# Performance work log

Measured on AMD Instinct MI355X. Metric: run time of the kernel, lower is better.

The kernel has to match this reference:

```python
import jax, jax.numpy as jnp
import numpy as np

B, N, NPOINT, NSAMPLE = 8, 8192, 2048, 32
RADIUS = 0.4
C_IN = 64
MLP = [64, 64, 128]
EPS = 1e-5
BIG = 1e10


def setup_inputs() -> dict:
    key = jax.random.key(0)
    ks = jax.random.split(key, 2 + 4 * len(MLP))
    inp = {
        'xyz': jax.random.normal(ks[0], (B, N, 3), jnp.float32),
        'features': jax.random.normal(ks[1], (B, C_IN, N), jnp.float32),
    }
    last_c = C_IN + 3
    j = 2
    for i, out_c in enumerate(MLP):
        inp[f'w{i}'] = jax.random.normal(ks[j], (out_c, last_c), jnp.float32) * (1.0 / np.sqrt(last_c)); j += 1
        inp[f'b{i}'] = jax.random.normal(ks[j], (out_c,), jnp.float32) * 0.01; j += 1
        inp[f'g{i}'] = 1.0 + 0.01 * jax.random.normal(ks[j], (out_c,), jnp.float32); j += 1
        inp[f'bt{i}'] = 0.01 * jax.random.normal(ks[j], (out_c,), jnp.float32); j += 1
        last_c = out_c
    return inp


def fps(xyz, m):
    # Farthest point sampling; deterministic start at index 0 (torch uses randint).
    b, n, _ = xyz.shape

    def step(carry, _):
        dist, far = carry
        centroid = jnp.take_along_axis(xyz, far[:, None, None], axis=1)  # [B,1,3]
        d = jnp.sum((xyz - centroid) ** 2, axis=-1)                      # [B,N]
        dist = jnp.minimum(dist, d)
        new_far = jnp.argmax(dist, axis=1)
        return (dist, new_far), far

    init = (jnp.full((b, n), BIG, xyz.dtype), jnp.zeros((b,), jnp.int32))
    _, idxs = jax.lax.scan(step, init, None, length=m)
    return jnp.transpose(idxs)  # [B,m]


def ball_query(xyz, centroids, radius, k):
    # Euclidean cdist via the (a-b)^2 = a^2 + b^2 - 2ab expansion.
    x2 = jnp.sum(xyz * xyz, axis=-1)            # [B,N]
    c2 = jnp.sum(centroids * centroids, axis=-1)  # [B,M]
    d2 = c2[:, :, None] + x2[:, None, :] - 2.0 * jnp.einsum('bmd,bnd->bmn', centroids, xyz)
    d = jnp.sqrt(jnp.maximum(d2, 0.0))           # [B,M,N]
    dm = jnp.where(d <= radius, d, BIG)
    _, idx = jax.lax.top_k(-dm, k)               # k smallest distances
    return idx                                   # [B,M,K]


def gather_points(x, idx):
    # x: [B,N,C], idx: [B,M,K] -> [B,M,K,C]
    b = x.shape[0]
    return x[jnp.arange(b)[:, None, None], idx]


def reference(xyz, features, w0, b0, g0, bt0, w1, b1, g1, bt1, w2, b2, g2, bt2):
    idx = fps(xyz, NPOINT)                                   # [B,M]
    new_xyz = jnp.take_along_axis(xyz, idx[:, :, None], axis=1)  # [B,M,3]
    knn_idx = ball_query(xyz, new_xyz, RADIUS, NSAMPLE)      # [B,M,K]
    grouped_xyz = gather_points(xyz, knn_idx)                # [B,M,K,3]
    grouped_xyz_norm = grouped_xyz - new_xyz[:, :, None, :]
    grouped_feat = gather_points(jnp.transpose(features, (0, 2, 1)), knn_idx)  # [B,M,K,C]
    feat = jnp.concatenate([grouped_xyz_norm, grouped_feat], axis=-1)          # [B,M,K,C+3]

    for w, b, g, bt in ((w0, b0, g0, bt0), (w1, b1, g1, bt1), (w2, b2, g2, bt2)):
        feat = jnp.einsum('bmkc,oc->bmko', feat, w) + b      # 1x1 conv
        mu = jnp.mean(feat, axis=(0, 1, 2))                  # BN, training-mode batch stats
        var = jnp.mean((feat - mu) ** 2, axis=(0, 1, 2))
        feat = (feat - mu) * jax.lax.rsqrt(var + EPS) * g + bt
        feat = jax.nn.relu(feat)

    new_feat = jnp.max(feat, axis=2)                         # max over neighbors -> [B,M,C_out]
    return new_xyz, jnp.transpose(new_feat, (0, 2, 1))       # [B,M,3], [B,C_out,M]
```

## Files before the change

### kernel.cpp

```cpp
#include <hip/hip_runtime.h>
#include <hip/hip_bf16.h>
#include <stdint.h>

typedef unsigned short u16;
typedef unsigned int   u32;
typedef unsigned long long u64;
typedef float v2f __attribute__((ext_vector_type(2)));
typedef __attribute__((ext_vector_type(8))) short bf16x8;
typedef __attribute__((ext_vector_type(4))) float f32x4;

#define B_    8
#define N_    8192
#define M_    2048
#define NS_   32
#define CIN_  64
#define ROWS_ (B_*M_*NS_)
#define BIGF  1e10f
#define EPSF  1e-5f
#define INV_ROWS (1.0f/524288.0f)

__device__ __forceinline__ u16 f2bf(float f){
  u32 x=__float_as_uint(f);
  return (u16)((x + 0x7FFFu + ((x>>16)&1u))>>16);
}
__device__ __forceinline__ float bf2f(u16 u){ return __uint_as_float(((u32)u)<<16); }

__device__ __forceinline__ u64 wave_max_key(u64 k){
#define DPP_LVL(CTRL) { \
    u32 lo_=(u32)__builtin_amdgcn_update_dpp(0,(int)(u32)k,(CTRL),0xF,0xF,true); \
    u32 hi_=(u32)__builtin_amdgcn_update_dpp(0,(int)(u32)(k>>32),(CTRL),0xF,0xF,true); \
    u64 o_=((u64)hi_<<32)|(u64)lo_; \
    k=(o_>k)?o_:k; }
  DPP_LVL(0x111)
  DPP_LVL(0x112)
  DPP_LVL(0x114)
  DPP_LVL(0x118)
  DPP_LVL(0x142)
  DPP_LVL(0x143)
#undef DPP_LVL
  return k;
}

__global__ __launch_bounds__(256) void k_prep(
    const float* w0,const float* b0,const float* g0,const float* bt0,
    const float* w1,const float* b1,const float* g1,const float* bt1,
    const float* w2,const float* b2,const float* g2,const float* bt2,
    float* biasf,float* gf,float* btf,float* stats,
    u16* Wb0h, u16* Wb0l, u16* Wb1h, u16* Wb1l, u16* Wb2h, u16* Wb2l)
{
  int tid=threadIdx.x;
  for (int i=tid;i<768;i+=256) stats[i]=0.f;
  for (int i=tid;i<6144;i+=256){
    int e=i&7, lane=(i>>3)&63, idx=i>>9;
    int tn=idx/3, k0=idx%3;
    int col = tn*16 + (lane&15);
    int k   = k0*32 + ((lane>>4)&3)*8 + e;
    float v = 0.f;
    if (k < 64)            v = w0[col*67 + 3 + k];
    else if (k < 67)       v = w0[col*67 + (k-64)];
    u16 hib = f2bf(v);
    Wb0h[i] = hib;
    Wb0l[i] = f2bf(v - bf2f(hib));
  }
  for (int i=tid;i<4096;i+=256){
    int e=i&7, lane=(i>>3)&63, k0=(i>>9)&1, tn=i>>10;
    int col = tn*16 + (lane&15);
    int k   = k0*32 + ((lane>>4)&3)*8 + e;
    float v = w1[col*64 + k];
    u16 hib = f2bf(v);
    Wb1h[i] = hib;
    Wb1l[i] = f2bf(v - bf2f(hib));
  }
  for (int i=tid;i<8192;i+=256){
    int e=i&7, lane=(i>>3)&63, k0=(i>>9)&1, tn=i>>10;
    int col = tn*16 + (lane&15);
    int k   = k0*32 + ((lane>>4)&3)*8 + e;
    float v = w2[col*64 + k];
    u16 hib = f2bf(v);
    Wb2h[i] = hib;
    Wb2l[i] = f2bf(v - bf2f(hib));
  }
  if (tid<64){
    biasf[0*128+tid]=b0[tid]; gf[0*128+tid]=g0[tid]; btf[0*128+tid]=bt0[tid];
    biasf[1*128+tid]=b1[tid]; gf[1*128+tid]=g1[tid]; btf[1*128+tid]=bt1[tid];
  }
  if (tid<128){
    biasf[2*128+tid]=b2[tid]; gf[2*128+tid]=g2[tid]; btf[2*128+tid]=bt2[tid];
  }
}

__global__ __launch_bounds__(512) void k_fpstr(const float* __restrict__ xyz,
                                               float* __restrict__ nxyz, float* __restrict__ out0,
                                               const float* __restrict__ feats, u16* __restrict__ featT)
{
#pragma clang fp contract(off)
  __shared__ float sx[N_], sy[N_], sz[N_];
  __shared__ int sidx[M_];
  __shared__ u64 skey[2][8];
  int tid=threadIdx.x;
  if (blockIdx.x >= 8){
    float (*t)[65] = (float(*)[65])sx;
    int idx = blockIdx.x - 8;
    int bb = idx >> 7, n0 = (idx & 127) * 64;
    int a=tid&63, q=tid>>6;
    const float* fp = feats + (size_t)bb*CIN_*N_;
    #pragma unroll
    for (int s=0;s<8;s++){ int c=q*8+s; t[c][a]=fp[(size_t)c*N_ + n0 + a]; }
    __syncthreads();
    u16* op = featT + (size_t)bb*N_*CIN_;
    #pragma unroll
    for (int s=0;s<8;s++){ int n=q*8+s; op[(size_t)(n0+n)*CIN_ + a] = f2bf(t[a][n]); }
    return;
  }
  int b=blockIdx.x;
  const float* xp = xyz + (size_t)b*N_*3;
  for (int i=tid;i<N_;i+=512){ sx[i]=xp[i*3]; sy[i]=xp[i*3+1]; sz[i]=xp[i*3+2]; }
  __syncthreads();
  v2f px[8],py[8],pz[8],md[8];
  int base = tid*16;
  #pragma unroll
  for (int p=0;p<8;p++){
    px[p]=*(const v2f*)&sx[base+2*p];
    py[p]=*(const v2f*)&sy[base+2*p];
    pz[p]=*(const v2f*)&sz[base+2*p];
    v2f m0; m0[0]=BIGF; m0[1]=BIGF; md[p]=m0;
  }
  u32 invb = 0xFFFFFFFFu - (u32)base;
  int far=0;
  int lane=tid&63, wv=tid>>6;
  for (int step=0; step<M_; step++){
    if (tid==0) sidx[step]=far;
    float cxs=sx[far], cys=sy[far], czs=sz[far];
    v2f cx; cx[0]=cxs; cx[1]=cxs;
    v2f cy; cy[0]=cys; cy[1]=cys;
    v2f cz; cz[0]=czs; cz[1]=czs;
    u64 kb=0;
    #pragma unroll
    for (int p=0;p<8;p++){
      v2f dx=px[p]-cx, dy=py[p]-cy, dz=pz[p]-cz;
      v2f d=(dx*dx+dy*dy)+dz*dz;
      v2f m=__builtin_elementwise_min(md[p],d);
      md[p]=m;
      u64 k0=((u64)__float_as_uint(m[0])<<32)|(u64)(invb-(u32)(2*p));
      u64 k1=((u64)__float_as_uint(m[1])<<32)|(u64)(invb-(u32)(2*p+1));
      u64 kp=(k1>k0)?k1:k0;
      kb=(kp>kb)?kp:kb;
    }
    kb = wave_max_key(kb);
    int par = step & 1;
    if (lane==63) skey[par][wv]=kb;
    __syncthreads();
    u64 a0=skey[par][0],a1=skey[par][1],a2=skey[par][2],a3=skey[par][3];
    u64 a4=skey[par][4],a5=skey[par][5],a6=skey[par][6],a7=skey[par][7];
    a0=(a1>a0)?a1:a0; a2=(a3>a2)?a3:a2; a4=(a5>a4)?a5:a4; a6=(a7>a6)?a7:a6;
    a0=(a2>a0)?a2:a0; a4=(a6>a4)?a6:a4;
    a0=(a4>a0)?a4:a0;
    far = (int)(0xFFFFFFFFu - (u32)(a0 & 0xFFFFFFFFull));
  }
  for (int i=tid;i<M_;i+=512){
    int id = sidx[i];
    float x=sx[id], y=sy[id], z=sz[id];
    size_t o=(size_t)(b*M_+i)*3;
    nxyz[o]=x; nxyz[o+1]=y; nxyz[o+2]=z;
    out0[o]=x; out0[o+1]=y; out0[o+2]=z;
  }
}

#define BQCAP 512
__global__ __launch_bounds__(512) void k_bq(const float* __restrict__ xyz, const float* __restrict__ nxyz,
                                            int* __restrict__ knn)
{
  __shared__ float4 sP[N_];
  __shared__ float candd[8][BQCAP];
  __shared__ u16  candi[8][BQCAP];
  int tid=threadIdx.x;
  int cid0 = blockIdx.x*8;
  int b = cid0 >> 11;
  const float* xp = xyz + (size_t)b*N_*3;
  for (int i=tid;i<N_;i+=512){
    float x=xp[i*3], y=xp[i*3+1], z=xp[i*3+2];
    float x2 = __fmul_rn(x,x);
    x2 = __fadd_rn(x2, __fmul_rn(y,y));
    x2 = __fadd_rn(x2, __fmul_rn(z,z));
    sP[i]=make_float4(x,y,z,x2);
  }
  __syncthreads();
  int w=tid>>6, lane=tid&63;
  int cid = cid0 + w;
  float cx=nxyz[(size_t)cid*3], cy=nxyz[(size_t)cid*3+1], cz=nxyz[(size_t)cid*3+2];
  float c2 = __fmul_rn(cx,cx);
  c2 = __fadd_rn(c2, __fmul_rn(cy,cy));
  c2 = __fadd_rn(c2, __fmul_rn(cz,cz));
  int cnt=0;
  for (int i0=0;i0<N_;i0+=64){
    int i=i0+lane;
    float4 p=sP[i];
    float dot = __fmul_rn(cx,p.x);
    dot = __fadd_rn(dot, __fmul_rn(cy,p.y));
    dot = __fadd_rn(dot, __fmul_rn(cz,p.z));
    float d2 = __fsub_rn(__fadd_rn(c2,p.w), __fmul_rn(2.0f,dot));
    float d = sqrtf(fmaxf(d2,0.f));
    bool in = (d <= 0.4f);
    u64 msk = __ballot(in);
    int pos = cnt + __popcll(msk & ((1ull<<lane)-1ull));
    if (in && pos<BQCAP){ candd[w][pos]=d; candi[w][pos]=(u16)i; }
    cnt += __popcll(msk);
  }
  int R = cnt<BQCAP ? cnt : BQCAP;
  int* kout = knn + (size_t)cid*NS_;
  if (R >= NS_){
    for (int s=0;s<NS_;s++){
      u64 kb = ~0ull;
      for (int j=lane;j<R;j+=64){
        float v=candd[w][j];
        u64 k = ((u64)__float_as_uint(v)<<32) | (u64)(u32)j;
        kb = (k<kb)?k:kb;
      }
      u64 inv = wave_max_key(~kb);
      if (lane==63){
        u64 kw = ~inv;
        int bpp = (int)(u32)(kw & 0xFFFFFFFFull);
        kout[s]=candi[w][bpp];
        candd[w][bpp]=3e38f;
      }
    }
  } else {
    if (lane<R) kout[lane]=candi[w][lane];
    int need = NS_-R, slot = R;
    for (int i0=0; i0<N_ && need>0; i0+=64){
      int i=i0+lane;
      float4 p=sP[i];
      float dot = __fmul_rn(cx,p.x);
      dot = __fadd_rn(dot, __fmul_rn(cy,p.y));
      dot = __fadd_rn(dot, __fmul_rn(cz,p.z));
      float d2 = __fsub_rn(__fadd_rn(c2,p.w), __fmul_rn(2.0f,dot));
      float d = sqrtf(fmaxf(d2,0.f));
      bool in = (d <= 0.4f);
      u64 mm = __ballot(!in);
      while (mm && need>0){
        int bpos = __ffsll((long long)mm)-1;
        if (lane==0) kout[slot] = i0+bpos;
        slot++; need--;
        mm &= mm-1;
      }
    }
  }
}

__global__ __launch_bounds__(256) void k_mm0(const float* __restrict__ xyz, const u16* __restrict__ featT,
                                             const int* __restrict__ knn, const float* __restrict__ nxyz,
                                             const u16* __restrict__ Wb0h, const u16* __restrict__ Wb0l,
                                             const float* __restrict__ bias0, u16* __restrict__ Y0)
{
  __shared__ u16 Xs[64*128];
  __shared__ u16 WH[12*64*8];
  __shared__ u16 WL[12*64*8];
  int tid=threadIdx.x;
  {
    const uint4* s4=(const uint4*)Wb0h; uint4* d4=(uint4*)WH;
    const uint4* s5=(const uint4*)Wb0l; uint4* d5=(uint4*)WL;
    for (int i=tid;i<768;i+=256){ d4[i]=s4[i]; d5[i]=s5[i]; }
  }
  size_t base=(size_t)blockIdx.x*64;
  {
    int rl=tid>>2, t=tid&3;
    int row=(int)base+rl;
    int bm = row>>5, b = row>>16;
    int n  = knn[row];
    const uint4* fp = (const uint4*)(featT + ((size_t)b*N_ + n)*CIN_);
    char* xr = (char*)Xs + rl*256;
    u32 swz = (u32)((rl&7)<<4);
    uint4 v0=fp[t*2], v1=fp[t*2+1];
    *(uint4*)(xr + ((t*32)    ^ swz)) = v0;
    *(uint4*)(xr + ((t*32+16) ^ swz)) = v1;
    uint4 pz = make_uint4(0u,0u,0u,0u);
    if (t==0){
      const float* cp = nxyz + (size_t)bm*3;
      const float* xp = xyz + ((size_t)b*N_ + n)*3;
      u32 w01 = (u32)f2bf(xp[0]-cp[0]) | ((u32)f2bf(xp[1]-cp[1])<<16);
      u32 w2  = (u32)f2bf(xp[2]-cp[2]);
      pz.x = w01; pz.y = w2;
    }
    *(uint4*)(xr + ((128+t*16) ^ swz)) = pz;
  }
  __syncthreads();
  int w=tid>>6, lane=tid&63;
  f32x4 acc[4];
  #pragma unroll
  for (int tn=0;tn<4;tn++){ acc[tn][0]=0.f; acc[tn][1]=0.f; acc[tn][2]=0.f; acc[tn][3]=0.f; }
  int arow = w*16 + (lane&15);
  u32 aswz = (u32)((arow&7)<<4);
  #pragma unroll
  for (int k0=0;k0<3;k0++){
    int aoff = arow*256 + (int)(((u32)((k0*32 + ((lane>>4)&3)*8)*2)) ^ aswz);
    bf16x8 a = *(const bf16x8*)((const char*)Xs + aoff);
    #pragma unroll
    for (int tn=0;tn<4;tn++){
      bf16x8 bl = *(const bf16x8*)&WL[((tn*3+k0)*64+lane)*8];
      bf16x8 bh = *(const bf16x8*)&WH[((tn*3+k0)*64+lane)*8];
      acc[tn] = __builtin_amdgcn_mfma_f32_16x16x32_bf16(a, bl, acc[tn], 0,0,0);
      acc[tn] = __builtin_amdgcn_mfma_f32_16x16x32_bf16(a, bh, acc[tn], 0,0,0);
    }
  }
  #pragma unroll
  for (int tn=0;tn<4;tn++){
    int col = tn*16 + (lane&15);
    float bb = bias0[col];
    #pragma unroll
    for (int j=0;j<4;j++){
      int row = w*16 + (lane>>4)*4 + j;
      Y0[(base+row)*64 + col] = f2bf(acc[tn][j] + bb);
    }
  }
}

template<int C>
__global__ __launch_bounds__(256) void k_stats(const u16* __restrict__ Y, float* __restrict__ statsOut)
{
  __shared__ float sred[4][128];
  int tid=threadIdx.x;
  int c0=(tid&7)*8;
  int rg=tid>>3;
  float s[8], ss[8];
  #pragma unroll
  for (int k=0;k<8;k++){ s[k]=0.f; ss[k]=0.f; }
  for (size_t r=(size_t)blockIdx.x*32+rg; r<ROWS_; r+=(size_t)gridDim.x*32){
    uint4 v=*(const uint4*)&Y[r*64+c0];
    u32 a[4]={v.x,v.y,v.z,v.w};
    #pragma unroll
    for (int q=0;q<4;q++){
      float lo=bf2f((u16)(a[q]&0xFFFFu));
      float hi=bf2f((u16)(a[q]>>16));
      s[q*2]+=lo;   ss[q*2]+=lo*lo;
      s[q*2+1]+=hi; ss[q*2+1]+=hi*hi;
    }
  }
  #pragma unroll
  for (int off=32; off>=8; off>>=1){
    #pragma unroll
    for (int k=0;k<8;k++){
      s[k]+=__shfl_down(s[k],off);
      ss[k]+=__shfl_down(ss[k],off);
    }
  }
  int lane=tid&63, wv=tid>>6;
  if (lane<8){
    #pragma unroll
    for (int k=0;k<8;k++){
      int ch=lane*8+k;
      sred[wv][ch]=s[k];
      sred[wv][64+ch]=ss[k];
    }
  }
  __syncthreads();
  if (tid<128){
    float a=sred[0][tid]+sred[1][tid]+sred[2][tid]+sred[3][tid];
    int ch=tid&63, which=tid>>6;
    atomicAdd(&statsOut[ch*2+which], a);
  }
}

__global__ __launch_bounds__(256) void k_mm1(u16* __restrict__ Y,
                                             const u16* __restrict__ Wb1h, const u16* __restrict__ Wb1l,
                                             const float* __restrict__ bias1, const float* __restrict__ gf0,
                                             const float* __restrict__ btf0, const float* __restrict__ stats0)
{
  __shared__ u16 Xs[64*64];
  __shared__ u16 WH[8*64*8];
  __shared__ u16 WL[8*64*8];
  __shared__ float sc[64], sh[64];
  int tid=threadIdx.x;
  if (tid<64){
    float mu = stats0[tid*2]*INV_ROWS;
    float var= stats0[tid*2+1]*INV_ROWS - mu*mu;
    float rs = 1.0f/sqrtf(var+EPSF);
    float s  = rs*gf0[tid];
    sc[tid]=s; sh[tid]=btf0[tid]-mu*s;
  }
  {
    const uint4* sh4=(const uint4*)Wb1h; uint4* dh4=(uint4*)WH;
    const uint4* sl4=(const uint4*)Wb1l; uint4* dl4=(uint4*)WL;
    dh4[tid]=sh4[tid]; dh4[tid+256]=sh4[tid+256];
    dl4[tid]=sl4[tid]; dl4[tid+256]=sl4[tid+256];
  }
  __syncthreads();
  size_t base=(size_t)blockIdx.x*64;
  for (int i=tid;i<512;i+=256){
    int rl=i>>3, c0=(i&7)*8;
    uint4 v=*(const uint4*)(Y + (base+rl)*64 + c0);
    u32 arr[4]={v.x,v.y,v.z,v.w};
    u32 pk[4];
    #pragma unroll
    for (int q=0;q<4;q++){
      int cc=c0+q*2;
      float lo=bf2f((u16)(arr[q]&0xFFFFu));
      float hi=bf2f((u16)(arr[q]>>16));
      lo=fmaxf(0.f, lo*sc[cc]+sh[cc]);
      hi=fmaxf(0.f, hi*sc[cc+1]+sh[cc+1]);
      pk[q] = (u32)f2bf(lo) | ((u32)f2bf(hi)<<16);
    }
    uint4 o4; o4.x=pk[0]; o4.y=pk[1]; o4.z=pk[2]; o4.w=pk[3];
    int byteoff = rl*128 + ((c0*2) ^ ((rl&7)<<4));
    *(uint4*)((char*)Xs + byteoff) = o4;
  }
  __syncthreads();
  int w=tid>>6, lane=tid&63;
  f32x4 acc[4];
  #pragma unroll
  for (int tn=0;tn<4;tn++){ acc[tn][0]=0.f; acc[tn][1]=0.f; acc[tn][2]=0.f; acc[tn][3]=0.f; }
  int arow = w*16 + (lane&15);
  #pragma unroll
  for (int k0=0;k0<2;k0++){
    int aoff = arow*128 + ((k0*64 + (lane>>4)*16) ^ ((arow&7)<<4));
    bf16x8 a = *(const bf16x8*)((const char*)Xs + aoff);
    #pragma unroll
    for (int tn=0;tn<4;tn++){
      bf16x8 bl = *(const bf16x8*)&WL[((tn*2+k0)*64+lane)*8];
      bf16x8 bh = *(const bf16x8*)&WH[((tn*2+k0)*64+lane)*8];
      acc[tn] = __builtin_amdgcn_mfma_f32_16x16x32_bf16(a, bl, acc[tn], 0,0,0);
      acc[tn] = __builtin_amdgcn_mfma_f32_16x16x32_bf16(a, bh, acc[tn], 0,0,0);
    }
  }
  #pragma unroll
  for (int tn=0;tn<4;tn++){
    int col = tn*16 + (lane&15);
    float bb = bias1[col];
    #pragma unroll
    for (int j=0;j<4;j++){
      int row = w*16 + (lane>>4)*4 + j;
      Y[(base+row)*64 + col] = f2bf(acc[tn][j] + bb);
    }
  }
}

__global__ __launch_bounds__(256) void k_mm2a(const u16* __restrict__ Y1,
                                              const u16* __restrict__ Wb2h, const u16* __restrict__ Wb2l,
                                              const float* __restrict__ bias2, const float* __restrict__ gf1,
                                              const float* __restrict__ btf1, const float* __restrict__ stats1,
                                              float* __restrict__ stats2, float* __restrict__ out1)
{
  __shared__ u16 Xs[64*64];
  __shared__ u16 WH[8192];
  __shared__ u16 WL[8192];
  __shared__ float Ys[64*128];
  __shared__ float sc[64], sh[64];
  __shared__ float sred[512];
  int tid=threadIdx.x;
  if (tid<64){
    float mu = stats1[tid*2]*INV_ROWS;
    float var= stats1[tid*2+1]*INV_ROWS - mu*mu;
    float rs = 1.0f/sqrtf(var+EPSF);
    float s  = rs*gf1[tid];
    sc[tid]=s; sh[tid]=btf1[tid]-mu*s;
  }
  {
    const uint4* s4=(const uint4*)Wb2h; uint4* d4=(uint4*)WH;
    const uint4* s5=(const uint4*)Wb2l; uint4* d5=(uint4*)WL;
    for (int i=tid;i<1024;i+=256){ d4[i]=s4[i]; d5[i]=s5[i]; }
  }
  int w=tid>>6, lane=tid&63;
  int pg=tid>>7, po=tid&127;
  float accSum=0.f, accSq=0.f;
  __syncthreads();
  for (int tile=blockIdx.x; tile<8192; tile+=gridDim.x){
    size_t base=(size_t)tile*64;
    for (int i=tid;i<512;i+=256){
      int rl=i>>3, c0=(i&7)*8;
      uint4 v=*(const uint4*)(Y1 + (base+rl)*64 + c0);
      u32 arr[4]={v.x,v.y,v.z,v.w};
      u32 pk[4];
      #pragma unroll
      for (int q=0;q<4;q++){
        int cc=c0+q*2;
        float lo=bf2f((u16)(arr[q]&0xFFFFu));
        float hi=bf2f((u16)(arr[q]>>16));
        lo=fmaxf(0.f, lo*sc[cc]+sh[cc]);
        hi=fmaxf(0.f, hi*sc[cc+1]+sh[cc+1]);
        pk[q] = (u32)f2bf(lo) | ((u32)f2bf(hi)<<16);
      }
      uint4 o4; o4.x=pk[0]; o4.y=pk[1]; o4.z=pk[2]; o4.w=pk[3];
      int byteoff = rl*128 + ((c0*2) ^ ((rl&7)<<4));
      *(uint4*)((char*)Xs + byteoff) = o4;
    }
    __syncthreads();
    f32x4 acc[8];
    #pragma unroll
    for (int tn=0;tn<8;tn++){ acc[tn][0]=0.f; acc[tn][1]=0.f; acc[tn][2]=0.f; acc[tn][3]=0.f; }
    int arow = w*16 + (lane&15);
    #pragma unroll
    for (int k0=0;k0<2;k0++){
      int aoff = arow*128 + ((k0*64 + (lane>>4)*16) ^ ((arow&7)<<4));
      bf16x8 a = *(const bf16x8*)((const char*)Xs + aoff);
      #pragma unroll
      for (int tn=0;tn<8;tn++){
        bf16x8 bl = *(const bf16x8*)&WL[((tn*2+k0)*64+lane)*8];
        bf16x8 bh = *(const bf16x8*)&WH[((tn*2+k0)*64+lane)*8];
        acc[tn] = __builtin_amdgcn_mfma_f32_16x16x32_bf16(a, bl, acc[tn], 0,0,0);
        acc[tn] = __builtin_amdgcn_mfma_f32_16x16x32_bf16(a, bh, acc[tn], 0,0,0);
      }
    }
    #pragma unroll
    for (int tn=0;tn<8;tn++){
      int col = tn*16 + (lane&15);
      float bb = bias2[col];
      #pragma unroll
      for (int j=0;j<4;j++){
        int row = w*16 + (lane>>4)*4 + j;
        int byteoff = row*512 + ((col*4) ^ ((row&7)<<4));
        *(float*)((char*)Ys + byteoff) = acc[tn][j] + bb;
      }
    }
    __syncthreads();
    {
      float mx=-3e38f;
      #pragma unroll 4
      for (int k=0;k<32;k++){
        int row = pg*32 + k;
        int byteoff = row*512 + ((po*4) ^ ((row&7)<<4));
        float y = *(const float*)((const char*)Ys + byteoff);
        accSum += y; accSq += y*y;
        mx = fmaxf(mx, y);
      }
      int bm = tile*2 + pg; int bi = bm>>11, m = bm&2047;
      out1[((size_t)bi*128+po)*M_ + m] = mx;
    }
    __syncthreads();
  }
  sred[tid]      = accSum;
  sred[256+tid]  = accSq;
  __syncthreads();
  if (tid<128){
    float s = sred[tid] + sred[tid+128];
    float q = sred[256+tid] + sred[256+tid+128];
    atomicAdd(&stats2[tid*2],   s);
    atomicAdd(&stats2[tid*2+1], q);
  }
}

__global__ __launch_bounds__(256) void k_pool(float* __restrict__ out1, const float* __restrict__ stats2,
                                              const float* __restrict__ gf2, const float* __restrict__ btf2)
{
  int idx = blockIdx.x*256 + threadIdx.x;
  int o = (idx >> 11) & 127;
  float mu = stats2[o*2]*INV_ROWS;
  float var= stats2[o*2+1]*INV_ROWS - mu*mu;
  float rs = 1.0f/sqrtf(var+EPSF);
  float s  = rs*gf2[o];
  float sh = btf2[o]-mu*s;
  out1[idx] = fmaxf(0.f, out1[idx]*s + sh);
}

extern "C" void kernel_launch(void* const* d_in, const int* in_sizes, int n_in,
                              void* d_out, int out_size, void* d_ws, size_t ws_size,
                              hipStream_t stream)
{
  (void)in_sizes; (void)n_in; (void)out_size; (void)ws_size;
  const float* xyz =(const float*)d_in[0];
  const float* feat=(const float*)d_in[1];
  const float* w0=(const float*)d_in[2],  *b0=(const float*)d_in[3],  *g0=(const float*)d_in[4],  *bt0=(const float*)d_in[5];
  const float* w1=(const float*)d_in[6],  *b1=(const float*)d_in[7],  *g1=(const float*)d_in[8],  *bt1=(const float*)d_in[9];
  const float* w2=(const float*)d_in[10], *b2=(const float*)d_in[11], *g2=(const float*)d_in[12], *bt2=(const float*)d_in[13];
  float* out0=(float*)d_out;
  float* out1=out0 + (size_t)B_*M_*3;

  char* ws=(char*)d_ws;
  float* nxyz =(float*)(ws);
  u16*   Wb1h =(u16*)  (ws + 196608);
  u16*   Wb1l =(u16*)  (ws + 204800);
  u16*   Wb2h =(u16*)  (ws + 212992);
  u16*   Wb2l =(u16*)  (ws + 229376);
  int*   knn  =(int*)  (ws + 262144);
  u16*   Wb0h =(u16*)  (ws + 2359296);
  u16*   Wb0l =(u16*)  (ws + 2376704);
  float* biasf=(float*)(ws + 2425856);
  float* gfp  =(float*)(ws + 2427392);
  float* btfp =(float*)(ws + 2428928);
  float* stats=(float*)(ws + 2430464);
  u16*   featT=(u16*)  (ws + 2433536);
  u16*   Y0   =(u16*)  (ws + 10822144);

  k_prep<<<1,256,0,stream>>>(w0,b0,g0,bt0,w1,b1,g1,bt1,w2,b2,g2,bt2,biasf,gfp,btfp,stats,
                             Wb0h,Wb0l,Wb1h,Wb1l,Wb2h,Wb2l);
  k_fpstr<<<8+1024,512,0,stream>>>(xyz, nxyz, out0, feat, featT);
  k_bq<<<2048,512,0,stream>>>(xyz, nxyz, knn);
  k_mm0<<<8192,256,0,stream>>>(xyz, featT, knn, nxyz, Wb0h, Wb0l, biasf+0, Y0);
  k_stats<64><<<128,256,0,stream>>>(Y0, stats+0);
  k_mm1<<<8192,256,0,stream>>>(Y0, Wb1h, Wb1l, biasf+128, gfp+0, btfp+0, stats+0);
  k_stats<64><<<128,256,0,stream>>>(Y0, stats+256);
  k_mm2a<<<512,256,0,stream>>>(Y0, Wb2h, Wb2l, biasf+256, gfp+128, btfp+128, stats+256, stats+512, out1);
  k_pool<<<8192,256,0,stream>>>(out1, stats+512, gfp+256, btfp+256);
}
```

Baseline: 2.323 ms.

## Fuse BN stats into matmul kernels, persistent grids, drop LDS staging in ball query

The two standalone batch-norm statistics kernels are removed. Their per-channel sum and sum-of-squares are now accumulated in the epilogues of k_mm0 and k_mm1, which become persistent 512-block grids looping over tiles, with shared-memory then global atomics for the totals. This saves two full re-reads of the intermediate activation buffer and two launches. Separately, k_bq no longer stages all 8192 points in LDS and instead reads xyz directly from global memory, recomputing |p|^2 per point. That lowers LDS use and may raise occupancy, at the cost of uncoalesced stride-3 global loads in the hot loop.

Measured after the change: 2.186 ms. 1.06x faster.

```diff
diff --git a/kernel.cpp b/kernel.cpp
--- a/kernel.cpp
+++ b/kernel.cpp
@@ -170,21 +170,12 @@
 __global__ __launch_bounds__(512) void k_bq(const float* __restrict__ xyz, const float* __restrict__ nxyz,
                                             int* __restrict__ knn)
 {
-  __shared__ float4 sP[N_];
   __shared__ float candd[8][BQCAP];
   __shared__ u16  candi[8][BQCAP];
   int tid=threadIdx.x;
   int cid0 = blockIdx.x*8;
   int b = cid0 >> 11;
   const float* xp = xyz + (size_t)b*N_*3;
-  for (int i=tid;i<N_;i+=512){
-    float x=xp[i*3], y=xp[i*3+1], z=xp[i*3+2];
-    float x2 = __fmul_rn(x,x);
-    x2 = __fadd_rn(x2, __fmul_rn(y,y));
-    x2 = __fadd_rn(x2, __fmul_rn(z,z));
-    sP[i]=make_float4(x,y,z,x2);
-  }
-  __syncthreads();
   int w=tid>>6, lane=tid&63;
   int cid = cid0 + w;
   float cx=nxyz[(size_t)cid*3], cy=nxyz[(size_t)cid*3+1], cz=nxyz[(size_t)cid*3+2];
@@ -194,11 +185,14 @@
   int cnt=0;
   for (int i0=0;i0<N_;i0+=64){
     int i=i0+lane;
-    float4 p=sP[i];
-    float dot = __fmul_rn(cx,p.x);
-    dot = __fadd_rn(dot, __fmul_rn(cy,p.y));
-    dot = __fadd_rn(dot, __fmul_rn(cz,p.z));
-    float d2 = __fsub_rn(__fadd_rn(c2,p.w), __fmul_rn(2.0f,dot));
+    float x=xp[i*3], y=xp[i*3+1], z=xp[i*3+2];
+    float pw = __fmul_rn(x,x);
+    pw = __fadd_rn(pw, __fmul_rn(y,y));
+    pw = __fadd_rn(pw, __fmul_rn(z,z));
+    float dot = __fmul_rn(cx,x);
+    dot = __fadd_rn(dot, __fmul_rn(cy,y));
+    dot = __fadd_rn(dot, __fmul_rn(cz,z));
+    float d2 = __fsub_rn(__fadd_rn(c2,pw), __fmul_rn(2.0f,dot));
     float d = sqrtf(fmaxf(d2,0.f));
     bool in = (d <= 0.4f);
     u64 msk = __ballot(in);
@@ -229,11 +223,14 @@
     int need = NS_-R, slot = R;
     for (int i0=0; i0<N_ && need>0; i0+=64){
       int i=i0+lane;
-      float4 p=sP[i];
-      float dot = __fmul_rn(cx,p.x);
-      dot = __fadd_rn(dot, __fmul_rn(cy,p.y));
-      dot = __fadd_rn(dot, __fmul_rn(cz,p.z));
-      float d2 = __fsub_rn(__fadd_rn(c2,p.w), __fmul_rn(2.0f,dot));
+      float x=xp[i*3], y=xp[i*3+1], z=xp[i*3+2];
+      float pw = __fmul_rn(x,x);
+      pw = __fadd_rn(pw, __fmul_rn(y,y));
+      pw = __fadd_rn(pw, __fmul_rn(z,z));
+      float dot = __fmul_rn(cx,x);
+      dot = __fadd_rn(dot, __fmul_rn(cy,y));
+      dot = __fadd_rn(dot, __fmul_rn(cz,z));
+      float d2 = __fsub_rn(__fadd_rn(c2,pw), __fmul_rn(2.0f,dot));
       float d = sqrtf(fmaxf(d2,0.f));
       bool in = (d <= 0.4f);
       u64 mm = __ballot(!in);
@@ -250,125 +247,103 @@
 __global__ __launch_bounds__(256) void k_mm0(const float* __restrict__ xyz, const u16* __restrict__ featT,
                                              const int* __restrict__ knn, const float* __restrict__ nxyz,
                                              const u16* __restrict__ Wb0h, const u16* __restrict__ Wb0l,
-                                             const float* __restrict__ bias0, u16* __restrict__ Y0)
+                                             const float* __restrict__ bias0, u16* __restrict__ Y0,
+                                             float* __restrict__ stats0)
 {
   __shared__ u16 Xs[64*128];
   __shared__ u16 WH[12*64*8];
   __shared__ u16 WL[12*64*8];
+  __shared__ float cs[128];
   int tid=threadIdx.x;
   {
     const uint4* s4=(const uint4*)Wb0h; uint4* d4=(uint4*)WH;
     const uint4* s5=(const uint4*)Wb0l; uint4* d5=(uint4*)WL;
     for (int i=tid;i<768;i+=256){ d4[i]=s4[i]; d5[i]=s5[i]; }
   }
-  size_t base=(size_t)blockIdx.x*64;
-  {
-    int rl=tid>>2, t=tid&3;
-    int row=(int)base+rl;
-    int bm = row>>5, b = row>>16;
-    int n  = knn[row];
-    const uint4* fp = (const uint4*)(featT + ((size_t)b*N_ + n)*CIN_);
-    char* xr = (char*)Xs + rl*256;
-    u32 swz = (u32)((rl&7)<<4);
-    uint4 v0=fp[t*2], v1=fp[t*2+1];
-    *(uint4*)(xr + ((t*32)    ^ swz)) = v0;
-    *(uint4*)(xr + ((t*32+16) ^ swz)) = v1;
-    uint4 pz = make_uint4(0u,0u,0u,0u);
-    if (t==0){
-      const float* cp = nxyz + (size_t)bm*3;
-      const float* xp = xyz + ((size_t)b*N_ + n)*3;
-      u32 w01 = (u32)f2bf(xp[0]-cp[0]) | ((u32)f2bf(xp[1]-cp[1])<<16);
-      u32 w2  = (u32)f2bf(xp[2]-cp[2]);
-      pz.x = w01; pz.y = w2;
-    }
-    *(uint4*)(xr + ((128+t*16) ^ swz)) = pz;
-  }
-  __syncthreads();
+  for (int i=tid;i<128;i+=256) cs[i]=0.f;
   int w=tid>>6, lane=tid&63;
-  f32x4 acc[4];
-  #pragma unroll
-  for (int tn=0;tn<4;tn++){ acc[tn][0]=0.f; acc[tn][1]=0.f; acc[tn][2]=0.f; acc[tn][3]=0.f; }
-  int arow = w*16 + (lane&15);
-  u32 aswz = (u32)((arow&7)<<4);
-  #pragma unroll
-  for (int k0=0;k0<3;k0++){
-    int aoff = arow*256 + (int)(((u32)((k0*32 + ((lane>>4)&3)*8)*2)) ^ aswz);
-    bf16x8 a = *(const bf16x8*)((const char*)Xs + aoff);
+  int rl=tid>>2, t=tid&3;
+  float sSum[4]={0.f,0.f,0.f,0.f}, sSq[4]={0.f,0.f,0.f,0.f};
+  __syncthreads();
+  for (int tile=blockIdx.x; tile<8192; tile+=gridDim.x){
+    size_t base=(size_t)tile*64;
+    {
+      int row=(int)base+rl;
+      int bm = row>>5, b = row>>16;
+      int n  = knn[row];
+      const uint4* fp = (const uint4*)(featT + ((size_t)b*N_ + n)*CIN_);
+      char* xr = (char*)Xs + rl*256;
+      u32 swz = (u32)((rl&7)<<4);
+      uint4 v0=fp[t*2], v1=fp[t*2+1];
+      *(uint4*)(xr + ((t*32)    ^ swz)) = v0;
+      *(uint4*)(xr + ((t*32+16) ^ swz)) = v1;
+      uint4 pz = make_uint4(0u,0u,0u,0u);
+      if (t==0){
+        const float* cp = nxyz + (size_t)bm*3;
+        const float* xp = xyz + ((size_t)b*N_ + n)*3;
+        u32 w01 = (u32)f2bf(xp[0]-cp[0]) | ((u32)f2bf(xp[1]-cp[1])<<16);
+        u32 w2  = (u32)f2bf(xp[2]-cp[2]);
+        pz.x = w01; pz.y = w2;
+      }
+      *(uint4*)(xr + ((128+t*16) ^ swz)) = pz;
+    }
+    __syncthreads();
+    f32x4 acc[4];
+    #pragma unroll
+    for (int tn=0;tn<4;tn++){ acc[tn][0]=0.f; acc[tn][1]=0.f; acc[tn][2]=0.f; acc[tn][3]=0.f; }
+    int arow = w*16 + (lane&15);
+    u32 aswz = (u32)((arow&7)<<4);
+    #pragma unroll
+    for (int k0=0;k0<3;k0++){
+      int aoff = arow*256 + (int)(((u32)((k0*32 + ((lane>>4)&3)*8)*2)) ^ aswz);
+      bf16x8 a = *(const bf16x8*)((const char*)Xs + aoff);
+      #pragma unroll
+      for (int tn=0;tn<4;tn++){
+        bf16x8 bl = *(const bf16x8*)&WL[((tn*3+k0)*64+lane)*8];
+        bf16x8 bh = *(const bf16x8*)&WH[((tn*3+k0)*64+lane)*8];
+        acc[tn] = __builtin_amdgcn_mfma_f32_16x16x32_bf16(a, bl, acc[tn], 0,0,0);
+        acc[tn] = __builtin_amdgcn_mfma_f32_16x16x32_bf16(a, bh, acc[tn], 0,0,0);
+      }
+    }
     #pragma unroll
     for (int tn=0;tn<4;tn++){
-      bf16x8 bl = *(const bf16x8*)&WL[((tn*3+k0)*64+lane)*8];
-      bf16x8 bh = *(const bf16x8*)&WH[((tn*3+k0)*64+lane)*8];
-      acc[tn] = __builtin_amdgcn_mfma_f32_16x16x32_bf16(a, bl, acc[tn], 0,0,0);
-      acc[tn] = __builtin_amdgcn_mfma_f32_16x16x32_bf16(a, bh, acc[tn], 0,0,0);
-    }
+      int col = tn*16 + (lane&15);
+      float bb = bias0[col];
+      #pragma unroll
+      for (int j=0;j<4;j++){
+        int row = w*16 + (lane>>4)*4 + j;
+        u16 yb = f2bf(acc[tn][j] + bb);
+        Y0[(base+row)*64 + col] = yb;
+        float yv = bf2f(yb);
+        sSum[tn]+=yv; sSq[tn]+=yv*yv;
+      }
+    }
+    __syncthreads();
   }
   #pragma unroll
   for (int tn=0;tn<4;tn++){
     int col = tn*16 + (lane&15);
-    float bb = bias0[col];
-    #pragma unroll
-    for (int j=0;j<4;j++){
-      int row = w*16 + (lane>>4)*4 + j;
-      Y0[(base+row)*64 + col] = f2bf(acc[tn][j] + bb);
-    }
-  }
-}
-
-template<int C>
-__global__ __launch_bounds__(256) void k_stats(const u16* __restrict__ Y, float* __restrict__ statsOut)
-{
-  __shared__ float sred[4][128];
-  int tid=threadIdx.x;
-  int c0=(tid&7)*8;
-  int rg=tid>>3;
-  float s[8], ss[8];
-  #pragma unroll
-  for (int k=0;k<8;k++){ s[k]=0.f; ss[k]=0.f; }
-  for (size_t r=(size_t)blockIdx.x*32+rg; r<ROWS_; r+=(size_t)gridDim.x*32){
-    uint4 v=*(const uint4*)&Y[r*64+c0];
-    u32 a[4]={v.x,v.y,v.z,v.w};
-    #pragma unroll
-    for (int q=0;q<4;q++){
-      float lo=bf2f((u16)(a[q]&0xFFFFu));
-      float hi=bf2f((u16)(a[q]>>16));
-      s[q*2]+=lo;   ss[q*2]+=lo*lo;
-      s[q*2+1]+=hi; ss[q*2+1]+=hi*hi;
-    }
-  }
-  #pragma unroll
-  for (int off=32; off>=8; off>>=1){
-    #pragma unroll
-    for (int k=0;k<8;k++){
-      s[k]+=__shfl_down(s[k],off);
-      ss[k]+=__shfl_down(ss[k],off);
-    }
-  }
-  int lane=tid&63, wv=tid>>6;
-  if (lane<8){
-    #pragma unroll
-    for (int k=0;k<8;k++){
-      int ch=lane*8+k;
-      sred[wv][ch]=s[k];
-      sred[wv][64+ch]=ss[k];
-    }
-  }
-  __syncthreads();
-  if (tid<128){
-    float a=sred[0][tid]+sred[1][tid]+sred[2][tid]+sred[3][tid];
-    int ch=tid&63, which=tid>>6;
-    atomicAdd(&statsOut[ch*2+which], a);
+    atomicAdd(&cs[col],    sSum[tn]);
+    atomicAdd(&cs[64+col], sSq[tn]);
+  }
+  __syncthreads();
+  if (tid<64){
+    atomicAdd(&stats0[tid*2],   cs[tid]);
+    atomicAdd(&stats0[tid*2+1], cs[64+tid]);
   }
 }
 
 __global__ __launch_bounds__(256) void k_mm1(u16* __restrict__ Y,
                                              const u16* __restrict__ Wb1h, const u16* __restrict__ Wb1l,
                                              const float* __restrict__ bias1, const float* __restrict__ gf0,
-                                             const float* __restrict__ btf0, const float* __restrict__ stats0)
+                                             const float* __restrict__ btf0, const float* __restrict__ stats0,
+                                             float* __restrict__ stats1)
 {
   __shared__ u16 Xs[64*64];
   __shared__ u16 WH[8*64*8];
   __shared__ u16 WL[8*64*8];
   __shared__ float sc[64], sh[64];
+  __shared__ float cs[128];
   int tid=threadIdx.x;
   if (tid<64){
     float mu = stats0[tid*2]*INV_ROWS;
@@ -383,53 +358,72 @@
     dh4[tid]=sh4[tid]; dh4[tid+256]=sh4[tid+256];
     dl4[tid]=sl4[tid]; dl4[tid+256]=sl4[tid+256];
   }
-  __syncthreads();
-  size_t base=(size_t)blockIdx.x*64;
-  for (int i=tid;i<512;i+=256){
-    int rl=i>>3, c0=(i&7)*8;
-    uint4 v=*(const uint4*)(Y + (base+rl)*64 + c0);
-    u32 arr[4]={v.x,v.y,v.z,v.w};
-    u32 pk[4];
-    #pragma unroll
-    for (int q=0;q<4;q++){
-      int cc=c0+q*2;
-      float lo=bf2f((u16)(arr[q]&0xFFFFu));
-      float hi=bf2f((u16)(arr[q]>>16));
-      lo=fmaxf(0.f, lo*sc[cc]+sh[cc]);
-      hi=fmaxf(0.f, hi*sc[cc+1]+sh[cc+1]);
-      pk[q] = (u32)f2bf(lo) | ((u32)f2bf(hi)<<16);
-    }
-    uint4 o4; o4.x=pk[0]; o4.y=pk[1]; o4.z=pk[2]; o4.w=pk[3];
-    int byteoff = rl*128 + ((c0*2) ^ ((rl&7)<<4));
-    *(uint4*)((char*)Xs + byteoff) = o4;
-  }
-  __syncthreads();
+  for (int i=tid;i<128;i+=256) cs[i]=0.f;
   int w=tid>>6, lane=tid&63;
-  f32x4 acc[4];
-  #pragma unroll
-  for (int tn=0;tn<4;tn++){ acc[tn][0]=0.f; acc[tn][1]=0.f; acc[tn][2]=0.f; acc[tn][3]=0.f; }
-  int arow = w*16 + (lane&15);
-  #pragma unroll
-  for (int k0=0;k0<2;k0++){
-    int aoff = arow*128 + ((k0*64 + (lane>>4)*16) ^ ((arow&7)<<4));
-    bf16x8 a = *(const bf16x8*)((const char*)Xs + aoff);
+  float sSum[4]={0.f,0.f,0.f,0.f}, sSq[4]={0.f,0.f,0.f,0.f};
+  __syncthreads();
+  for (int tile=blockIdx.x; tile<8192; tile+=gridDim.x){
+    size_t base=(size_t)tile*64;
+    for (int i=tid;i<512;i+=256){
+      int rl=i>>3, c0=(i&7)*8;
+      uint4 v=*(const uint4*)(Y + (base+rl)*64 + c0);
+      u32 arr[4]={v.x,v.y,v.z,v.w};
+      u32 pk[4];
+      #pragma unroll
+      for (int q=0;q<4;q++){
+        int cc=c0+q*2;
+        float lo=bf2f((u16)(arr[q]&0xFFFFu));
+        float hi=bf2f((u16)(arr[q]>>16));
+        lo=fmaxf(0.f, lo*sc[cc]+sh[cc]);
+        hi=fmaxf(0.f, hi*sc[cc+1]+sh[cc+1]);
+        pk[q] = (u32)f2bf(lo) | ((u32)f2bf(hi)<<16);
+      }
+      uint4 o4; o4.x=pk[0]; o4.y=pk[1]; o4.z=pk[2]; o4.w=pk[3];
+      int byteoff = rl*128 + ((c0*2) ^ ((rl&7)<<4));
+      *(uint4*)((char*)Xs + byteoff) = o4;
+    }
+    __syncthreads();
+    f32x4 acc[4];
+    #pragma unroll
+    for (int tn=0;tn<4;tn++){ acc[tn][0]=0.f; acc[tn][1]=0.f; acc[tn][2]=0.f; acc[tn][3]=0.f; }
+    int arow = w*16 + (lane&15);
+    #pragma unroll
+    for (int k0=0;k0<2;k0++){
+      int aoff = arow*128 + ((k0*64 + (lane>>4)*16) ^ ((arow&7)<<4));
+      bf16x8 a = *(const bf16x8*)((const char*)Xs + aoff);
+      #pragma unroll
+      for (int tn=0;tn<4;tn++){
+        bf16x8 bl = *(const bf16x8*)&WL[((tn*2+k0)*64+lane)*8];
+        bf16x8 bh = *(const bf16x8*)&WH[((tn*2+k0)*64+lane)*8];
+        acc[tn] = __builtin_amdgcn_mfma_f32_16x16x32_bf16(a, bl, acc[tn], 0,0,0);
+        acc[tn] = __builtin_amdgcn_mfma_f32_16x16x32_bf16(a, bh, acc[tn], 0,0,0);
+      }
+    }
     #pragma unroll
     for (int tn=0;tn<4;tn++){
-      bf16x8 bl = *(const bf16x8*)&WL[((tn*2+k0)*64+lane)*8];
-      bf16x8 bh = *(const bf16x8*)&WH[((tn*2+k0)*64+lane)*8];
-      acc[tn] = __builtin_amdgcn_mfma_f32_16x16x32_bf16(a, bl, acc[tn], 0,0,0);
-      acc[tn] = __builtin_amdgcn_mfma_f32_16x16x32_bf16(a, bh, acc[tn], 0,0,0);
-    }
+      int col = tn*16 + (lane&15);
+      float bb = bias1[col];
+      #pragma unroll
+      for (int j=0;j<4;j++){
+        int row = w*16 + (lane>>4)*4 + j;
+        u16 yb = f2bf(acc[tn][j] + bb);
+        Y[(base+row)*64 + col] = yb;
+        float yv = bf2f(yb);
+        sSum[tn]+=yv; sSq[tn]+=yv*yv;
+      }
+    }
+    __syncthreads();
   }
   #pragma unroll
   for (int tn=0;tn<4;tn++){
     int col = tn*16 + (lane&15);
-    float bb = bias1[col];
-    #pragma unroll
-    for (int j=0;j<4;j++){
-      int row = w*16 + (lane>>4)*4 + j;
-      Y[(base+row)*64 + col] = f2bf(acc[tn][j] + bb);
-    }
+    atomicAdd(&cs[col],    sSum[tn]);
+    atomicAdd(&cs[64+col], sSq[tn]);
+  }
+  __syncthreads();
+  if (tid<64){
+    atomicAdd(&stats1[tid*2],   cs[tid]);
+    atomicAdd(&stats1[tid*2+1], cs[64+tid]);
   }
 }
 
@@ -583,10 +577,8 @@
                              Wb0h,Wb0l,Wb1h,Wb1l,Wb2h,Wb2l);
   k_fpstr<<<8+1024,512,0,stream>>>(xyz, nxyz, out0, feat, featT);
   k_bq<<<2048,512,0,stream>>>(xyz, nxyz, knn);
-  k_mm0<<<8192,256,0,stream>>>(xyz, featT, knn, nxyz, Wb0h, Wb0l, biasf+0, Y0);
-  k_stats<64><<<128,256,0,stream>>>(Y0, stats+0);
-  k_mm1<<<8192,256,0,stream>>>(Y0, Wb1h, Wb1l, biasf+128, gfp+0, btfp+0, stats+0);
-  k_stats<64><<<128,256,0,stream>>>(Y0, stats+256);
+  k_mm0<<<512,256,0,stream>>>(xyz, featT, knn, nxyz, Wb0h, Wb0l, biasf+0, Y0, stats+0);
+  k_mm1<<<512,256,0,stream>>>(Y0, Wb1h, Wb1l, biasf+128, gfp+0, btfp+0, stats+0, stats+256);
   k_mm2a<<<512,256,0,stream>>>(Y0, Wb2h, Wb2l, biasf+256, gfp+128, btfp+128, stats+256, stats+512, out1);
   k_pool<<<8192,256,0,stream>>>(out1, stats+512, gfp+256, btfp+256);
 }
```
